# Kernel tuning notes

Hardware: AMD Instinct MI355X
Metric: run time of the kernel (lower is better)

Reference implementation:

```python
import jax, jax.numpy as jnp
import numpy as np

N = 1024     # natom
DH = 31      # node feature dim (h)
DE = 16      # edge feature dim (e)
H1 = 64      # MLP hidden width
T = 3        # timesteps (hard-coded in module)
DIN = 2 * (DH + 1) + DE  # MLP input dim = 80


def _mlp(x, W0, b0, W1, b1, W2, b2):
    # MLP_flax with layers [64, 64, 1]: Dense+relu, Dense+relu, Dense
    x = jax.nn.relu(x @ W0 + b0)
    x = jax.nn.relu(x @ W1 + b1)
    return x @ W2 + b2


def setup_inputs() -> dict:
    key = jax.random.key(0)
    ks = jax.random.split(key, 10)
    h = jax.random.normal(ks[0], (N, DH), dtype=jnp.float32)
    e = jax.random.normal(ks[1], (N, N, DE), dtype=jnp.float32)
    q = jax.random.normal(ks[2], (N, 1), dtype=jnp.float32)
    # binary cutoff mask (float, as multiplied in the original)
    cutoff_mask = (jax.random.uniform(ks[3], (N, N)) < 0.5).astype(jnp.float32)
    s0 = 1.0 / np.sqrt(DIN)
    s1 = 1.0 / np.sqrt(H1)
    W0 = jax.random.normal(ks[4], (T, DIN, H1), dtype=jnp.float32) * s0
    b0 = jnp.zeros((T, H1), dtype=jnp.float32)
    W1 = jax.random.normal(ks[5], (T, H1, H1), dtype=jnp.float32) * s1
    b1 = jnp.zeros((T, H1), dtype=jnp.float32)
    W2 = jax.random.normal(ks[6], (T, H1, 1), dtype=jnp.float32) * s1
    b2 = jnp.zeros((T, 1), dtype=jnp.float32)
    return {"h": h, "e": e, "q": q, "cutoff_mask": cutoff_mask, "natom": N,
            "W0": W0, "b0": b0, "W1": W1, "b1": b1, "W2": W2, "b2": b2}


def reference(h, e, q, cutoff_mask, natom, W0, b0, W1, b1, W2, b2):
    for t in range(T):
        a = jnp.concatenate([h, q], axis=-1)             # [N, DH+1] per-atom input
        d = a.shape[-1]
        ai = jnp.broadcast_to(a[:, None, :], (natom, natom, d))  # inp_i[i,j] = a[i]
        aj = jnp.broadcast_to(a[None, :, :], (natom, natom, d))  # inp_j[i,j] = a[j]
        inp_ij = jnp.concatenate([ai, aj, e], axis=-1)   # [N, N, DIN]
        inp_ji = jnp.concatenate([aj, ai, e], axis=-1)   # [N, N, DIN]
        elec_ij = _mlp(inp_ij, W0[t], b0[t], W1[t], b1[t], W2[t], b2[t])[..., 0]  # [N, N]
        elec_ji = _mlp(inp_ji, W0[t], b0[t], W1[t], b1[t], W2[t], b2[t])[..., 0]  # [N, N]
        antisym = (elec_ij - elec_ji) * cutoff_mask
        q = q + jnp.sum(antisym, axis=1, keepdims=True)  # [N, 1]
    return q
```

## Files before the change

### kernel.cpp

```cpp
#include <hip/hip_runtime.h>


constexpr int Nn = 1024;

typedef _Float16 half4 __attribute__((ext_vector_type(4)));
typedef _Float16 half8 __attribute__((ext_vector_type(8)));
typedef __fp16   fp16x2 __attribute__((ext_vector_type(2)));
typedef float    f32x4 __attribute__((ext_vector_type(4)));
typedef unsigned int uint2v __attribute__((ext_vector_type(2)));
typedef unsigned int uint4v __attribute__((ext_vector_type(4)));

#define MFMAH32(A, B, C) __builtin_amdgcn_mfma_f32_16x16x32_f16(A, B, C, 0, 0, 0)

#if __has_builtin(__builtin_amdgcn_mfma_f32_16x16x16f16)
__device__ inline f32x4 mfma16(half4 a, half4 b, f32x4 c) {
    return __builtin_amdgcn_mfma_f32_16x16x16f16(a, b, c, 0, 0, 0);
}
#else
__device__ inline f32x4 mfma16(half4 a, half4 b, f32x4 c) {
    half8 a8 = {a[0], a[1], a[2], a[3], (_Float16)0, (_Float16)0, (_Float16)0, (_Float16)0};
    half8 b8 = {b[0], b[1], b[2], b[3], (_Float16)0, (_Float16)0, (_Float16)0, (_Float16)0};
    return MFMAH32(a8, b8, c);
}
#endif

__device__ inline unsigned int pkrtz(float a, float b) {
    fp16x2 r = __builtin_amdgcn_cvt_pkrtz(a, b);
    return __builtin_bit_cast(unsigned int, r);
}
__device__ inline f32x4 max0(f32x4 a) {
    f32x4 z = {0.f, 0.f, 0.f, 0.f};
    return __builtin_elementwise_max(a, z);
}

__global__ __launch_bounds__(256) void epn_frag_kernel(
    const float* __restrict__ W0,
    const float* __restrict__ W1,
    const float* __restrict__ b1,
    const float* __restrict__ W2,
    const float* __restrict__ qin,
    uint2v* __restrict__ fw0e,
    uint4*  __restrict__ fw1,
    float*  __restrict__ b1s,
    float*  __restrict__ w2s,
    float*  __restrict__ qout)
{
    const int idx = blockIdx.x * 256 + threadIdx.x;
    if (idx < 768) {
        int lane = idx & 63, t = (idx >> 6) & 3, ts = idx >> 8;
        int nl = lane & 15, qd = lane >> 4;
        float v[4];
        #pragma unroll
        for (int j = 0; j < 4; ++j)
            v[j] = W0[ts * 80 * 64 + (64 + qd * 4 + j) * 64 + t * 16 + nl] * 0.0625f;
        uint2v p = {pkrtz(v[0], v[1]), pkrtz(v[2], v[3])};
        fw0e[idx] = p;
    } else if (idx < 2304) {
        int i2 = idx - 768;
        int lane = i2 & 63, t2 = (i2 >> 6) & 3, sp = (i2 >> 8) & 1, ts = i2 >> 9;
        int nl = lane & 15, qd = lane >> 4;
        float v[8];
        #pragma unroll
        for (int j = 0; j < 8; ++j) {
            int k = (2 * (j >> 2) + sp) * 16 + qd * 4 + (j & 3);
            v[j] = W1[ts * 64 * 64 + k * 64 + t2 * 16 + nl];
        }
        uint4 p;
        p.x = pkrtz(v[0], v[1]); p.y = pkrtz(v[2], v[3]);
        p.z = pkrtz(v[4], v[5]); p.w = pkrtz(v[6], v[7]);
        fw1[(ts * 8 + sp * 4 + t2) * 64 + lane] = p;
    } else if (idx < 2496) {
        int i2 = idx - 2304;
        b1s[i2] = b1[i2] * 0.0625f;
        w2s[i2] = W2[i2] * 16.f;
    } else if (idx < 2752) {
        int i4 = idx - 2496;
        *(float4*)&qout[i4 * 4] = *(const float4*)&qin[i4 * 4];
    }
}

__global__ __launch_bounds__(256) void epn_proj_kernel(
    const float* __restrict__ h, const float* __restrict__ qcur,
    const float* __restrict__ W0, const float* __restrict__ b0,
    float* __restrict__ P, float* __restrict__ Q)
{
    __shared__ float sa[4][32];
    const int tid = threadIdx.x;
    const int base = blockIdx.x * 4;
    if (tid < 128) {
        int la = tid >> 5, c = tid & 31, atom = base + la;
        sa[la][c] = (c < 31) ? h[atom * 31 + c] : qcur[atom];
    }
    __syncthreads();
    const int la = tid >> 6, m = tid & 63, atom = base + la;
    float accP = b0[m], accQ = 0.f;
    #pragma unroll
    for (int c = 0; c < 32; ++c) {
        float av = sa[la][c];
        accP = fmaf(av, W0[c * 64 + m], accP);
        accQ = fmaf(av, W0[(32 + c) * 64 + m], accQ);
    }
    P[atom * 64 + m] = accP * 0.0625f;
    Q[atom * 64 + m] = accQ * 0.0625f;
}

__global__ __launch_bounds__(256, 4) void epn_main_kernel(
    const float* __restrict__ e, const float* __restrict__ mask,
    const float* __restrict__ Pg, const float* __restrict__ Qg,
    const uint2v* __restrict__ fragW0e,
    const uint4*  __restrict__ fragW1,
    const float* __restrict__ b1s, const float* __restrict__ w2s,
    float* __restrict__ qout)
{
    __shared__ float sPi[16][68], sQi[16][68];
    __shared__ float sPj[16][68], sQj[16][68];
    __shared__ float sb1[64], sw2[64];

    const int tid  = threadIdx.x;
    const int lane = tid & 63;
    const int wv   = tid >> 6;
    const int nl   = lane & 15;
    const int qd   = lane >> 4;
    const int i0   = blockIdx.y * 16;
    const int jb   = blockIdx.x * 64;

    const int sr = tid >> 4, sc4 = (tid & 15) * 4;
    *(float4*)&sPi[sr][sc4] = *(const float4*)&Pg[(i0 + sr) * 64 + sc4];
    *(float4*)&sQi[sr][sc4] = *(const float4*)&Qg[(i0 + sr) * 64 + sc4];
    *(float4*)&sPj[sr][sc4] = *(const float4*)&Pg[(jb + sr) * 64 + sc4];
    *(float4*)&sQj[sr][sc4] = *(const float4*)&Qg[(jb + sr) * 64 + sc4];
    if (tid < 64) { sb1[tid] = b1s[tid]; sw2[tid] = w2s[tid]; }

    uint2v Aw0e[4];
    #pragma unroll
    for (int t = 0; t < 4; ++t) Aw0e[t] = fragW0e[t * 64 + lane];
    uint4 w1r[8];
    #pragma unroll
    for (int i = 0; i < 8; ++i) w1r[i] = fragW1[i * 64 + lane];

    float4 eP = *(const float4*)(e + ((size_t)(i0 + wv * 4) * Nn + (jb + nl)) * 16 + qd * 4);
    float  mP = mask[(size_t)(i0 + wv * 4) * Nn + jb + nl];

    __syncthreads();

    for (int st = 0; st < 4; ++st) {
        float4 pjr, qjr;
        if (st < 3) {
            int jatom = jb + (st + 1) * 16 + sr;
            pjr = *(const float4*)&Pg[jatom * 64 + sc4];
            qjr = *(const float4*)&Qg[jatom * 64 + sc4];
        }

        #pragma unroll
        for (int g = 0; g < 4; ++g) {
            const int il = wv * 4 + g;
            float4 ec = eP; float mc = mP;
            const int gs = st * 4 + g;
            if (gs < 15) {
                int ngs = gs + 1, nst = ngs >> 2, ng = ngs & 3;
                int nil = wv * 4 + ng;
                eP = *(const float4*)(e + ((size_t)(i0 + nil) * Nn + (jb + nst * 16 + nl)) * 16 + qd * 4);
                mP = mask[(size_t)(i0 + nil) * Nn + jb + nst * 16 + nl];
            }

            uint2v ep = {pkrtz(ec.x, ec.y), pkrtz(ec.z, ec.w)};
            half4 Be = __builtin_bit_cast(half4, ep);

            uint4v bu[2], bv[2];
            #pragma unroll
            for (int t = 0; t < 4; ++t) {
                const int off = t * 16 + qd * 4;
                f32x4 Pi = *(const f32x4*)&sPi[il][off];
                f32x4 Qi = *(const f32x4*)&sQi[il][off];
                f32x4 Qj = *(const f32x4*)&sQj[nl][off];
                f32x4 Pj = *(const f32x4*)&sPj[nl][off];
                half4 aw = __builtin_bit_cast(half4, Aw0e[t]);
                f32x4 Eu = max0(mfma16(aw, Be, Pi + Qj));
                f32x4 Ev = max0(mfma16(aw, Be, Pj + Qi));
                const int sp = t & 1, b = (t >> 1) * 2;
                bu[sp][b]     = pkrtz(Eu[0], Eu[1]);
                bu[sp][b + 1] = pkrtz(Eu[2], Eu[3]);
                bv[sp][b]     = pkrtz(Ev[0], Ev[1]);
                bv[sp][b + 1] = pkrtz(Ev[2], Ev[3]);
            }

            f32x4 s4 = {0.f, 0.f, 0.f, 0.f};
            #pragma unroll
            for (int t2 = 0; t2 < 4; ++t2) {
                f32x4 binit = *(const f32x4*)&sb1[t2 * 16 + qd * 4];
                f32x4 w2q   = *(const f32x4*)&sw2[t2 * 16 + qd * 4];
                half8 w1a = __builtin_bit_cast(half8, w1r[t2]);
                half8 w1b = __builtin_bit_cast(half8, w1r[4 + t2]);
                f32x4 x = MFMAH32(w1a, __builtin_bit_cast(half8, bu[0]), binit);
                x = MFMAH32(w1b, __builtin_bit_cast(half8, bu[1]), x);
                f32x4 y = MFMAH32(w1a, __builtin_bit_cast(half8, bv[0]), binit);
                y = MFMAH32(w1b, __builtin_bit_cast(half8, bv[1]), y);
                s4 += (max0(x) - max0(y)) * w2q;
            }

            float s = ((s4[0] + s4[1]) + (s4[2] + s4[3])) * mc;
            s += __shfl_xor(s, 1);
            s += __shfl_xor(s, 2);
            s += __shfl_xor(s, 4);
            s += __shfl_xor(s, 8);
            s += __shfl_xor(s, 16);
            s += __shfl_xor(s, 32);
            if (lane == 0) atomicAdd(&qout[i0 + il], s);
        }

        if (st < 3) {
            __syncthreads();
            *(float4*)&sPj[sr][sc4] = pjr;
            *(float4*)&sQj[sr][sc4] = qjr;
            __syncthreads();
        }
    }
}

extern "C" void kernel_launch(void* const* d_in, const int* in_sizes, int n_in,
                              void* d_out, int out_size, void* d_ws, size_t ws_size,
                              hipStream_t stream) {
    const float* h    = (const float*)d_in[0];
    const float* e    = (const float*)d_in[1];
    const float* q    = (const float*)d_in[2];
    const float* mask = (const float*)d_in[3];
    const float* W0   = (const float*)d_in[5];
    const float* b0   = (const float*)d_in[6];
    const float* W1   = (const float*)d_in[7];
    const float* b1   = (const float*)d_in[8];
    const float* W2   = (const float*)d_in[9];

    float* qout = (float*)d_out;
    char*  ws   = (char*)d_ws;
    float*  Pws  = (float*)(ws);
    float*  Qws  = (float*)(ws + 256 * 1024);
    uint2v* fw0e = (uint2v*)(ws + 512 * 1024);
    uint4*  fw1  = (uint4*)(ws + 512 * 1024 + 6144);
    float*  b1s  = (float*)(ws + 512 * 1024 + 30720);
    float*  w2s  = (float*)(ws + 512 * 1024 + 31488);

    epn_frag_kernel<<<11, 256, 0, stream>>>(W0, W1, b1, W2, q, fw0e, fw1, b1s, w2s, qout);
    for (int t = 0; t < 3; ++t) {
        epn_proj_kernel<<<256, 256, 0, stream>>>(h, qout, W0 + t * 80 * 64, b0 + t * 64,
                                                 Pws, Qws);
        epn_main_kernel<<<dim3(16, 64), 256, 0, stream>>>(
            e, mask, Pws, Qws,
            fw0e + (size_t)t * 4 * 64, fw1 + (size_t)t * 8 * 64,
            b1s + t * 64, w2s + t * 64, qout);
    }
}
```

Baseline: 235.9 us.

## Precompute q-independent projections once and apply q correction inside main kernel

Precomputes the h-dependent parts of the first-layer projections for all three timesteps in one setup kernel, removing the per-step projection kernel launches. The main kernel now adds the q-dependent term (q times W0 rows 31/63) on the fly, with q rebuilt from the input plus per-step delta buffers, and a final kernel sums the deltas. The j-tile is also halved to 32 with twice as many blocks and occupancy hint raised to 8, which increases parallelism but duplicates i-side setup per block.

```diff
diff --git a/kernel.cpp b/kernel.cpp
--- a/kernel.cpp
+++ b/kernel.cpp
@@ -33,84 +33,93 @@
     return __builtin_elementwise_max(a, z);
 }
 
-__global__ __launch_bounds__(256) void epn_frag_kernel(
+__global__ __launch_bounds__(256) void epn_setup_kernel(
     const float* __restrict__ W0,
     const float* __restrict__ W1,
+    const float* __restrict__ b0,
     const float* __restrict__ b1,
     const float* __restrict__ W2,
-    const float* __restrict__ qin,
+    const float* __restrict__ h,
     uint2v* __restrict__ fw0e,
     uint4*  __restrict__ fw1,
     float*  __restrict__ b1s,
     float*  __restrict__ w2s,
-    float*  __restrict__ qout)
+    float*  __restrict__ w31s,
+    float*  __restrict__ w63s,
+    float*  __restrict__ Pb,
+    float*  __restrict__ Qb,
+    float*  __restrict__ D)
 {
-    const int idx = blockIdx.x * 256 + threadIdx.x;
-    if (idx < 768) {
-        int lane = idx & 63, t = (idx >> 6) & 3, ts = idx >> 8;
-        int nl = lane & 15, qd = lane >> 4;
-        float v[4];
+    const int b = blockIdx.x, tid = threadIdx.x;
+    if (b < 768) {
+        const int ts = b >> 8, base = (b & 255) * 4;
+        __shared__ float sa[4][32];
+        if (tid < 128) {
+            int la = tid >> 5, c = tid & 31;
+            sa[la][c] = (c < 31) ? h[(base + la) * 31 + c] : 0.f;
+        }
+        __syncthreads();
+        const int la = tid >> 6, m = tid & 63, atom = base + la;
+        const float* W0t = W0 + ts * 80 * 64;
+        float accP = b0[ts * 64 + m], accQ = 0.f;
         #pragma unroll
-        for (int j = 0; j < 4; ++j)
-            v[j] = W0[ts * 80 * 64 + (64 + qd * 4 + j) * 64 + t * 16 + nl] * 0.0625f;
-        uint2v p = {pkrtz(v[0], v[1]), pkrtz(v[2], v[3])};
-        fw0e[idx] = p;
-    } else if (idx < 2304) {
-        int i2 = idx - 768;
-        int lane = i2 & 63, t2 = (i2 >> 6) & 3, sp = (i2 >> 8) & 1, ts = i2 >> 9;
-        int nl = lane & 15, qd = lane >> 4;
-        float v[8];
-        #pragma unroll
-        for (int j = 0; j < 8; ++j) {
-            int k = (2 * (j >> 2) + sp) * 16 + qd * 4 + (j & 3);
-            v[j] = W1[ts * 64 * 64 + k * 64 + t2 * 16 + nl];
-        }
-        uint4 p;
-        p.x = pkrtz(v[0], v[1]); p.y = pkrtz(v[2], v[3]);
-        p.z = pkrtz(v[4], v[5]); p.w = pkrtz(v[6], v[7]);
-        fw1[(ts * 8 + sp * 4 + t2) * 64 + lane] = p;
-    } else if (idx < 2496) {
-        int i2 = idx - 2304;
-        b1s[i2] = b1[i2] * 0.0625f;
-        w2s[i2] = W2[i2] * 16.f;
-    } else if (idx < 2752) {
-        int i4 = idx - 2496;
-        *(float4*)&qout[i4 * 4] = *(const float4*)&qin[i4 * 4];
-    }
-}
-
-__global__ __launch_bounds__(256) void epn_proj_kernel(
-    const float* __restrict__ h, const float* __restrict__ qcur,
-    const float* __restrict__ W0, const float* __restrict__ b0,
-    float* __restrict__ P, float* __restrict__ Q)
-{
-    __shared__ float sa[4][32];
-    const int tid = threadIdx.x;
-    const int base = blockIdx.x * 4;
-    if (tid < 128) {
-        int la = tid >> 5, c = tid & 31, atom = base + la;
-        sa[la][c] = (c < 31) ? h[atom * 31 + c] : qcur[atom];
-    }
-    __syncthreads();
-    const int la = tid >> 6, m = tid & 63, atom = base + la;
-    float accP = b0[m], accQ = 0.f;
-    #pragma unroll
-    for (int c = 0; c < 32; ++c) {
-        float av = sa[la][c];
-        accP = fmaf(av, W0[c * 64 + m], accP);
-        accQ = fmaf(av, W0[(32 + c) * 64 + m], accQ);
-    }
-    P[atom * 64 + m] = accP * 0.0625f;
-    Q[atom * 64 + m] = accQ * 0.0625f;
-}
-
-__global__ __launch_bounds__(256, 4) void epn_main_kernel(
+        for (int c = 0; c < 31; ++c) {
+            float av = sa[la][c];
+            accP = fmaf(av, W0t[c * 64 + m], accP);
+            accQ = fmaf(av, W0t[(32 + c) * 64 + m], accQ);
+        }
+        Pb[((size_t)ts * Nn + atom) * 64 + m] = accP * 0.0625f;
+        Qb[((size_t)ts * Nn + atom) * 64 + m] = accQ * 0.0625f;
+    } else {
+        const int idx = (b - 768) * 256 + tid;
+        if (idx < 768) {
+            int lane = idx & 63, t = (idx >> 6) & 3, ts = idx >> 8;
+            int nl = lane & 15, qd = lane >> 4;
+            float v[4];
+            #pragma unroll
+            for (int j = 0; j < 4; ++j)
+                v[j] = W0[ts * 80 * 64 + (64 + qd * 4 + j) * 64 + t * 16 + nl] * 0.0625f;
+            uint2v p = {pkrtz(v[0], v[1]), pkrtz(v[2], v[3])};
+            fw0e[idx] = p;
+        } else if (idx < 2304) {
+            int i2 = idx - 768;
+            int lane = i2 & 63, t2 = (i2 >> 6) & 3, sp = (i2 >> 8) & 1, ts = i2 >> 9;
+            int nl = lane & 15, qd = lane >> 4;
+            float v[8];
+            #pragma unroll
+            for (int j = 0; j < 8; ++j) {
+                int k = (2 * (j >> 2) + sp) * 16 + qd * 4 + (j & 3);
+                v[j] = W1[ts * 64 * 64 + k * 64 + t2 * 16 + nl];
+            }
+            uint4 p;
+            p.x = pkrtz(v[0], v[1]); p.y = pkrtz(v[2], v[3]);
+            p.z = pkrtz(v[4], v[5]); p.w = pkrtz(v[6], v[7]);
+            fw1[(ts * 8 + sp * 4 + t2) * 64 + lane] = p;
+        } else if (idx < 2496) {
+            int i2 = idx - 2304;
+            b1s[i2] = b1[i2] * 0.0625f;
+            w2s[i2] = W2[i2] * 16.f;
+        } else if (idx < 2688) {
+            int i2 = idx - 2496;
+            int ts = i2 >> 6, c = i2 & 63;
+            w31s[i2] = W0[ts * 80 * 64 + 31 * 64 + c] * 0.0625f;
+            w63s[i2] = W0[ts * 80 * 64 + 63 * 64 + c] * 0.0625f;
+        } else if (idx < 3456) {
+            int i4 = idx - 2688;
+            *(float4*)&D[i4 * 4] = make_float4(0.f, 0.f, 0.f, 0.f);
+        }
+    }
+}
+
+__global__ __launch_bounds__(256, 8) void epn_main_kernel(
     const float* __restrict__ e, const float* __restrict__ mask,
-    const float* __restrict__ Pg, const float* __restrict__ Qg,
+    const float* __restrict__ Pb, const float* __restrict__ Qb,
     const uint2v* __restrict__ fragW0e,
     const uint4*  __restrict__ fragW1,
     const float* __restrict__ b1s, const float* __restrict__ w2s,
-    float* __restrict__ qout)
+    const float* __restrict__ w31s, const float* __restrict__ w63s,
+    const float* __restrict__ qin, const float* __restrict__ Dp0,
+    const float* __restrict__ Dp1, float* __restrict__ Dout, int tstep)
 {
     __shared__ float sPi[16][68], sQi[16][68];
     __shared__ float sPj[16][68], sQj[16][68];
@@ -122,13 +131,24 @@
     const int nl   = lane & 15;
     const int qd   = lane >> 4;
     const int i0   = blockIdx.y * 16;
-    const int jb   = blockIdx.x * 64;
-
-    const int sr = tid >> 4, sc4 = (tid & 15) * 4;
-    *(float4*)&sPi[sr][sc4] = *(const float4*)&Pg[(i0 + sr) * 64 + sc4];
-    *(float4*)&sQi[sr][sc4] = *(const float4*)&Qg[(i0 + sr) * 64 + sc4];
-    *(float4*)&sPj[sr][sc4] = *(const float4*)&Pg[(jb + sr) * 64 + sc4];
-    *(float4*)&sQj[sr][sc4] = *(const float4*)&Qg[(jb + sr) * 64 + sc4];
+    const int jb   = blockIdx.x * 32;
+    const int sr   = tid >> 4, sc4 = (tid & 15) * 4;
+
+    float qi = qin[i0 + sr], qj = qin[jb + sr];
+    if (tstep > 0) { qi += Dp0[i0 + sr]; qj += Dp0[jb + sr]; }
+    if (tstep > 1) { qi += Dp1[i0 + sr]; qj += Dp1[jb + sr]; }
+    {
+        f32x4 w31v = *(const f32x4*)&w31s[sc4];
+        f32x4 w63v = *(const f32x4*)&w63s[sc4];
+        f32x4 pbi = *(const f32x4*)&Pb[(i0 + sr) * 64 + sc4];
+        f32x4 qbi = *(const f32x4*)&Qb[(i0 + sr) * 64 + sc4];
+        f32x4 pbj = *(const f32x4*)&Pb[(jb + sr) * 64 + sc4];
+        f32x4 qbj = *(const f32x4*)&Qb[(jb + sr) * 64 + sc4];
+        *(f32x4*)&sPi[sr][sc4] = pbi + qi * w31v;
+        *(f32x4*)&sQi[sr][sc4] = qbi + qi * w63v;
+        *(f32x4*)&sPj[sr][sc4] = pbj + qj * w31v;
+        *(f32x4*)&sQj[sr][sc4] = qbj + qj * w63v;
+    }
     if (tid < 64) { sb1[tid] = b1s[tid]; sw2[tid] = w2s[tid]; }
 
     uint2v Aw0e[4];
@@ -143,12 +163,19 @@
 
     __syncthreads();
 
-    for (int st = 0; st < 4; ++st) {
-        float4 pjr, qjr;
-        if (st < 3) {
-            int jatom = jb + (st + 1) * 16 + sr;
-            pjr = *(const float4*)&Pg[jatom * 64 + sc4];
-            qjr = *(const float4*)&Qg[jatom * 64 + sc4];
+    for (int st = 0; st < 2; ++st) {
+        f32x4 pjn, qjn;
+        if (st == 0) {
+            int jatom = jb + 16 + sr;
+            float qn = qin[jatom];
+            if (tstep > 0) qn += Dp0[jatom];
+            if (tstep > 1) qn += Dp1[jatom];
+            f32x4 w31v = *(const f32x4*)&w31s[sc4];
+            f32x4 w63v = *(const f32x4*)&w63s[sc4];
+            f32x4 pbj = *(const f32x4*)&Pb[jatom * 64 + sc4];
+            f32x4 qbj = *(const f32x4*)&Qb[jatom * 64 + sc4];
+            pjn = pbj + qn * w31v;
+            qjn = qbj + qn * w63v;
         }
 
         #pragma unroll
@@ -156,7 +183,7 @@
             const int il = wv * 4 + g;
             float4 ec = eP; float mc = mP;
             const int gs = st * 4 + g;
-            if (gs < 15) {
+            if (gs < 7) {
                 int ngs = gs + 1, nst = ngs >> 2, ng = ngs & 3;
                 int nil = wv * 4 + ng;
                 eP = *(const float4*)(e + ((size_t)(i0 + nil) * Nn + (jb + nst * 16 + nl)) * 16 + qd * 4);
@@ -205,16 +232,24 @@
             s += __shfl_xor(s, 8);
             s += __shfl_xor(s, 16);
             s += __shfl_xor(s, 32);
-            if (lane == 0) atomicAdd(&qout[i0 + il], s);
-        }
-
-        if (st < 3) {
+            if (lane == 0) atomicAdd(&Dout[i0 + il], s);
+        }
+
+        if (st == 0) {
             __syncthreads();
-            *(float4*)&sPj[sr][sc4] = pjr;
-            *(float4*)&sQj[sr][sc4] = qjr;
+            *(f32x4*)&sPj[sr][sc4] = pjn;
+            *(f32x4*)&sQj[sr][sc4] = qjn;
             __syncthreads();
         }
     }
+}
+
+__global__ __launch_bounds__(256) void epn_final_kernel(
+    const float* __restrict__ qin, const float* __restrict__ D,
+    float* __restrict__ qout)
+{
+    int i = blockIdx.x * 256 + threadIdx.x;
+    qout[i] = qin[i] + D[i] + D[Nn + i] + D[2 * Nn + i];
 }
 
 extern "C" void kernel_launch(void* const* d_in, const int* in_sizes, int n_in,
@@ -232,20 +267,25 @@
 
     float* qout = (float*)d_out;
     char*  ws   = (char*)d_ws;
-    float*  Pws  = (float*)(ws);
-    float*  Qws  = (float*)(ws + 256 * 1024);
-    uint2v* fw0e = (uint2v*)(ws + 512 * 1024);
-    uint4*  fw1  = (uint4*)(ws + 512 * 1024 + 6144);
-    float*  b1s  = (float*)(ws + 512 * 1024 + 30720);
-    float*  w2s  = (float*)(ws + 512 * 1024 + 31488);
-
-    epn_frag_kernel<<<11, 256, 0, stream>>>(W0, W1, b1, W2, q, fw0e, fw1, b1s, w2s, qout);
+    float*  Pb   = (float*)(ws);
+    float*  Qb   = (float*)(ws + 786432);
+    uint2v* fw0e = (uint2v*)(ws + 1572864);
+    uint4*  fw1  = (uint4*)(ws + 1579008);
+    float*  b1s  = (float*)(ws + 1603584);
+    float*  w2s  = (float*)(ws + 1604352);
+    float*  w31s = (float*)(ws + 1605120);
+    float*  w63s = (float*)(ws + 1605888);
+    float*  D    = (float*)(ws + 1606656);
+
+    epn_setup_kernel<<<782, 256, 0, stream>>>(W0, W1, b0, b1, W2, h,
+                                              fw0e, fw1, b1s, w2s, w31s, w63s,
+                                              Pb, Qb, D);
     for (int t = 0; t < 3; ++t) {
-        epn_proj_kernel<<<256, 256, 0, stream>>>(h, qout, W0 + t * 80 * 64, b0 + t * 64,
-                                                 Pws, Qws);
-        epn_main_kernel<<<dim3(16, 64), 256, 0, stream>>>(
-            e, mask, Pws, Qws,
+        epn_main_kernel<<<dim3(32, 64), 256, 0, stream>>>(
+            e, mask, Pb + (size_t)t * Nn * 64, Qb + (size_t)t * Nn * 64,
             fw0e + (size_t)t * 4 * 64, fw1 + (size_t)t * 8 * 64,
-            b1s + t * 64, w2s + t * 64, qout);
-    }
-}
+            b1s + t * 64, w2s + t * 64, w31s + t * 64, w63s + t * 64,
+            q, D, D + Nn, D + (size_t)t * Nn, t);
+    }
+    epn_final_kernel<<<4, 256, 0, stream>>>(q, D, qout);
+}
```

New measurement: 694.5 us. 194% more time.
